# Kernel tuning notes

Hardware: AMD Instinct MI355X
Metric: run time of the kernel (lower is better)

The kernel has to match this reference:

```python
import jax, jax.numpy as jnp
import numpy as np

B, L, D = 16, 1024, 512
EPS = 1e-6


def setup_inputs() -> dict:
    key = jax.random.key(0)
    ks = jax.random.split(key, 12)
    inp = {
        'q': jax.random.normal(ks[0], (B, L, D), jnp.float32),
        'k': jax.random.normal(ks[1], (B, L, D), jnp.float32),
        'v': jax.random.normal(ks[2], (B, L, D), jnp.float32),
        'inputs_lengths': jax.random.randint(ks[3], (B,), 1, L + 1),
        'distance_matrix': jax.random.uniform(ks[4], (B, L, L), jnp.float32),
        'Wq': jax.random.normal(ks[5], (D, D), jnp.float32) / np.sqrt(D),
        'Wk': jax.random.normal(ks[6], (D, D), jnp.float32) / np.sqrt(D),
        'Wv': jax.random.normal(ks[7], (D, D), jnp.float32) / np.sqrt(D),
        'Wqt': jax.random.normal(ks[8], (D, D), jnp.float32) / np.sqrt(D),
        'Wkt': jax.random.normal(ks[9], (D, D), jnp.float32) / np.sqrt(D),
        'Wfc': jax.random.normal(ks[10], (D, D), jnp.float32) / np.sqrt(D),
        'gamma': jnp.ones((D,), jnp.float32),
        'beta': jnp.zeros((D,), jnp.float32),
    }
    return inp


def reference(q, k, v, inputs_lengths, distance_matrix, Wq, Wk, Wv, Wqt, Wkt, Wfc, gamma, beta):
    temperature = jnp.asarray(D, q.dtype) ** 0.5
    residual = q
    # projections (torch Linear: x @ W.T)
    qp = jnp.einsum('bld,ed->ble', q, Wq)
    kp = jnp.einsum('bld,ed->ble', k, Wk)
    vp = jnp.einsum('bld,ed->ble', v, Wv)
    qt = jnp.einsum('bld,ed->ble', q, Wqt)
    kt = jnp.einsum('bld,ed->ble', k, Wkt)
    # distance-weighted time features: [B,L,L] @ [B,L,D]
    qt = jnp.einsum('blm,bmd->bld', distance_matrix, qt)
    kt = jnp.einsum('blm,bmd->bld', distance_matrix, kt)
    # scores: content + distance term
    attn = jnp.einsum('bld,bmd->blm', qp / temperature, kp)
    attn = attn + jnp.einsum('bld,bmd->blm', qt / temperature, kt)
    # pad_zero_masking: zero out key positions beyond each sequence length
    mask = (jnp.arange(L)[None, :] < inputs_lengths[:, None]).astype(attn.dtype)  # [B, L]
    mask = mask[:, None, :]  # [B, 1, L] broadcast over query dim
    attn = jnp.tanh(attn * mask) * mask
    out = jnp.einsum('blm,bmd->bld', attn, vp)
    out = jnp.einsum('bld,ed->ble', out, Wfc) + residual
    # LayerNorm(eps=1e-6)
    mu = jnp.mean(out, axis=-1, keepdims=True)
    var = jnp.mean((out - mu) ** 2, axis=-1, keepdims=True)
    out = (out - mu) * jax.lax.rsqrt(var + EPS) * gamma + beta
    return (out, attn)
```

## Files before the change

kernel.cpp:

```cpp
#include <hip/hip_runtime.h>
#include <math.h>

#define LL 1024
#define DD 512
#define NB 16

typedef __attribute__((ext_vector_type(8))) short bf16x8;
typedef __attribute__((ext_vector_type(4))) float f32x4;
typedef unsigned short u16;
typedef unsigned int u32;
typedef const __attribute__((address_space(1))) void* gptr_t;
typedef __attribute__((address_space(3))) void* sptr_t;

static const long NLD = (long)NB * LL * DD;
static const long NLL = (long)NB * LL * LL;

__device__ __forceinline__ u16 f2bf(float x) {
  u32 u = __float_as_uint(x);
  u += 0x7fffu + ((u >> 16) & 1u);
  return (u16)(u >> 16);
}
__device__ __forceinline__ float bf2f(u16 h) {
  return __uint_as_float((u32)h << 16);
}

__global__ __launch_bounds__(256) void k_split3(
    const float* __restrict__ q, const float* __restrict__ k,
    const float* __restrict__ v, u16* __restrict__ qh, u16* __restrict__ ql,
    u16* __restrict__ kh, u16* __restrict__ kl, u16* __restrict__ vh) {
  const int z = blockIdx.z;
  const float* x = (z == 0) ? q : (z == 1) ? k : v;
  u16* hi = (z == 0) ? qh : (z == 1) ? kh : vh;
  u16* lo = (z == 0) ? ql : kl;
  const long stride = (long)gridDim.x * 1024;
  for (long i = ((long)blockIdx.x * 256 + threadIdx.x) * 4; i < NLD;
       i += stride) {
    const float4 vv = *(const float4*)(x + i);
    ushort4 h;
    h.x = f2bf(vv.x);
    h.y = f2bf(vv.y);
    h.z = f2bf(vv.z);
    h.w = f2bf(vv.w);
    *(ushort4*)(hi + i) = h;
    if (z < 2) {
      ushort4 s;
      s.x = f2bf(vv.x - bf2f(h.x));
      s.y = f2bf(vv.y - bf2f(h.y));
      s.z = f2bf(vv.z - bf2f(h.z));
      s.w = f2bf(vv.w - bf2f(h.w));
      *(ushort4*)(lo + i) = s;
    }
  }
}

__global__ __launch_bounds__(256) void k_splitd(const float* __restrict__ x,
                                                u16* __restrict__ hi,
                                                u16* __restrict__ lo) {
  const long stride = (long)gridDim.x * 1024;
  for (long i = ((long)blockIdx.x * 256 + threadIdx.x) * 4; i < NLL;
       i += stride) {
    const float4 v = *(const float4*)(x + i);
    ushort4 h, s;
    h.x = f2bf(v.x);
    h.y = f2bf(v.y);
    h.z = f2bf(v.z);
    h.w = f2bf(v.w);
    s.x = f2bf(v.x - bf2f(h.x));
    s.y = f2bf(v.y - bf2f(h.y));
    s.z = f2bf(v.z - bf2f(h.z));
    s.w = f2bf(v.w - bf2f(h.w));
    *(ushort4*)(hi + i) = h;
    *(ushort4*)(lo + i) = s;
  }
}

__global__ __launch_bounds__(256) void k_splitw(
    const float* __restrict__ Wq, const float* __restrict__ Wk,
    const float* __restrict__ Wv, const float* __restrict__ Wfc,
    const float* __restrict__ Wqt, const float* __restrict__ Wkt,
    u16* __restrict__ Wq_h, u16* __restrict__ Wk_h, u16* __restrict__ Wv_h,
    u16* __restrict__ Wfc_h, u16* __restrict__ Wqt_h,
    u16* __restrict__ Wqt_l, u16* __restrict__ Wkt_h,
    u16* __restrict__ Wkt_l) {
  const int z = blockIdx.z;
  const float* x;
  u16 *hi, *lo = nullptr;
  switch (z) {
    case 0: x = Wq; hi = Wq_h; break;
    case 1: x = Wk; hi = Wk_h; break;
    case 2: x = Wv; hi = Wv_h; break;
    case 3: x = Wfc; hi = Wfc_h; break;
    case 4: x = Wqt; hi = Wqt_h; lo = Wqt_l; break;
    default: x = Wkt; hi = Wkt_h; lo = Wkt_l; break;
  }
  const long i = ((long)blockIdx.x * 256 + threadIdx.x) * 4;
  const float4 v = *(const float4*)(x + i);
  ushort4 h;
  h.x = f2bf(v.x);
  h.y = f2bf(v.y);
  h.z = f2bf(v.z);
  h.w = f2bf(v.w);
  *(ushort4*)(hi + i) = h;
  if (z >= 4) {
    ushort4 s;
    s.x = f2bf(v.x - bf2f(h.x));
    s.y = f2bf(v.y - bf2f(h.y));
    s.z = f2bf(v.z - bf2f(h.z));
    s.w = f2bf(v.w - bf2f(h.w));
    *(ushort4*)(lo + i) = s;
  }
}

template <int NISS>
__device__ __forceinline__ void stage_tile(const u16* __restrict__ G, long ld,
                                           int row0, int k0, char* lds, int w,
                                           int l) {
#pragma unroll
  for (int i = 0; i < NISS; ++i) {
    const int off = i * 4096 + w * 1024 + l * 16;
    const int r = off >> 6;
    const int cp = (off >> 4) & 3;
    const int c = cp ^ ((r >> 1) & 3);
    __builtin_amdgcn_global_load_lds(
        (gptr_t)(G + (long)(row0 + r) * ld + k0 + c * 8),
        (sptr_t)(lds + i * 4096 + w * 1024), 16, 0, 0);
  }
}

__device__ __forceinline__ bf16x8 read_frag(const char* lds, int r, int ks) {
  const int cp = ks ^ ((r >> 1) & 3);
  return *(const bf16x8*)(lds + r * 64 + cp * 16);
}

__device__ __forceinline__ void core_plain(const u16* __restrict__ A, long lda,
                                           const u16* __restrict__ B, long ldb,
                                           int K, int bm, int bn, char* smem,
                                           f32x4 acc[4][4]) {
  const int tid = threadIdx.x, w = tid >> 6, l = tid & 63;
  const int wm = (w >> 1) * 64, wn = (w & 1) * 64;
  const int fr = l & 15, ks = l >> 4;
  char* As = smem;
  char* Bs = smem + 8192;
  for (int k0 = 0; k0 < K; k0 += 32) {
    stage_tile<2>(A, lda, bm, k0, As, w, l);
    stage_tile<2>(B, ldb, bn, k0, Bs, w, l);
    __syncthreads();
    bf16x8 af[4], bg[4];
#pragma unroll
    for (int i = 0; i < 4; ++i) {
      af[i] = read_frag(As, wm + i * 16 + fr, ks);
      bg[i] = read_frag(Bs, wn + i * 16 + fr, ks);
    }
#pragma unroll
    for (int mi = 0; mi < 4; ++mi)
#pragma unroll
      for (int ni = 0; ni < 4; ++ni)
        acc[mi][ni] = __builtin_amdgcn_mfma_f32_16x16x32_bf16(
            af[mi], bg[ni], acc[mi][ni], 0, 0, 0);
    __syncthreads();
  }
}

__device__ __forceinline__ void core_split(
    const u16* __restrict__ Ah, const u16* __restrict__ Al, long lda,
    const u16* __restrict__ Bh, const u16* __restrict__ Bl, long ldb, int K,
    int bm, int bn, char* smem, f32x4 acc[4][4]) {
  const int tid = threadIdx.x, w = tid >> 6, l = tid & 63;
  const int wm = (w >> 1) * 64, wn = (w & 1) * 64;
  const int fr = l & 15, ks = l >> 4;
  char* Ash = smem;
  char* Bsh = smem + 8192;
  char* Asl = smem + 16384;
  char* Bsl = smem + 24576;
  for (int k0 = 0; k0 < K; k0 += 32) {
    stage_tile<2>(Ah, lda, bm, k0, Ash, w, l);
    stage_tile<2>(Bh, ldb, bn, k0, Bsh, w, l);
    stage_tile<2>(Al, lda, bm, k0, Asl, w, l);
    stage_tile<2>(Bl, ldb, bn, k0, Bsl, w, l);
    __syncthreads();
    bf16x8 ah[4], bh[4];
#pragma unroll
    for (int i = 0; i < 4; ++i) {
      ah[i] = read_frag(Ash, wm + i * 16 + fr, ks);
      bh[i] = read_frag(Bsh, wn + i * 16 + fr, ks);
    }
#pragma unroll
    for (int mi = 0; mi < 4; ++mi)
#pragma unroll
      for (int ni = 0; ni < 4; ++ni)
        acc[mi][ni] = __builtin_amdgcn_mfma_f32_16x16x32_bf16(
            ah[mi], bh[ni], acc[mi][ni], 0, 0, 0);
    bf16x8 bl[4];
#pragma unroll
    for (int ni = 0; ni < 4; ++ni)
      bl[ni] = read_frag(Bsl, wn + ni * 16 + fr, ks);
#pragma unroll
    for (int mi = 0; mi < 4; ++mi)
#pragma unroll
      for (int ni = 0; ni < 4; ++ni)
        acc[mi][ni] = __builtin_amdgcn_mfma_f32_16x16x32_bf16(
            ah[mi], bl[ni], acc[mi][ni], 0, 0, 0);
    bf16x8 al[4];
#pragma unroll
    for (int mi = 0; mi < 4; ++mi)
      al[mi] = read_frag(Asl, wm + mi * 16 + fr, ks);
#pragma unroll
    for (int mi = 0; mi < 4; ++mi)
#pragma unroll
      for (int ni = 0; ni < 4; ++ni)
        acc[mi][ni] = __builtin_amdgcn_mfma_f32_16x16x32_bf16(
            al[mi], bh[ni], acc[mi][ni], 0, 0, 0);
    __syncthreads();
  }
}

#define EPI_PROLOG()                                       \
  const int tid = threadIdx.x, w = tid >> 6, l = tid & 63; \
  const int wm = (w >> 1) * 64, wn = (w & 1) * 64;         \
  const int fr = l & 15, ks = l >> 4;

__global__ __launch_bounds__(256, 3) void k_proj_p(
    const u16* __restrict__ q_hi, const u16* __restrict__ k_hi,
    const u16* __restrict__ v_hi, const u16* __restrict__ Wq_h,
    const u16* __restrict__ Wk_h, const u16* __restrict__ Wv_h,
    const int* __restrict__ lens, u16* __restrict__ qp, u16* __restrict__ kp,
    u16* __restrict__ vp) {
  const int bm = blockIdx.y * 128, bn = blockIdx.x * 128;
  const u16 *A, *B;
  u16* C;
  switch (blockIdx.z) {
    case 0: A = q_hi; B = Wq_h; C = qp; break;
    case 1: A = k_hi; B = Wk_h; C = kp; break;
    default: A = v_hi; B = Wv_h; C = vp; break;
  }
  if (blockIdx.z != 0) {
    const int len = lens[bm >> 10];
    if ((bm & 1023) >= len) return;
  }
  __shared__ __align__(16) char smem[16384];
  f32x4 acc[4][4] = {};
  core_plain(A, DD, B, DD, DD, bm, bn, smem, acc);
  EPI_PROLOG()
#pragma unroll
  for (int mi = 0; mi < 4; ++mi) {
    const int R0 = bm + wm + mi * 16 + ks * 4;
#pragma unroll
    for (int ni = 0; ni < 4; ++ni) {
      const int col = bn + wn + ni * 16 + fr;
#pragma unroll
      for (int j = 0; j < 4; ++j)
        C[(long)(R0 + j) * DD + col] = f2bf(acc[mi][ni][j]);
    }
  }
}

__global__ __launch_bounds__(256, 3) void k_proj_t(
    const u16* __restrict__ q_hi, const u16* __restrict__ q_lo,
    const u16* __restrict__ k_hi, const u16* __restrict__ k_lo,
    const u16* __restrict__ Wqt_h, const u16* __restrict__ Wqt_l,
    const u16* __restrict__ Wkt_h, const u16* __restrict__ Wkt_l,
    u16* __restrict__ qt0h, u16* __restrict__ qt0l, u16* __restrict__ kt0h,
    u16* __restrict__ kt0l) {
  const int sel = blockIdx.z;
  const u16* Ah = sel ? k_hi : q_hi;
  const u16* Al = sel ? k_lo : q_lo;
  const u16* Bh = sel ? Wkt_h : Wqt_h;
  const u16* Bl = sel ? Wkt_l : Wqt_l;
  u16* Ch = sel ? kt0h : qt0h;
  u16* Cl = sel ? kt0l : qt0l;
  __shared__ __align__(16) char smem[32768];
  const int bm = blockIdx.y * 128, bn = blockIdx.x * 128;
  f32x4 acc[4][4] = {};
  core_split(Ah, Al, DD, Bh, Bl, DD, DD, bm, bn, smem, acc);
  EPI_PROLOG()
#pragma unroll
  for (int mi = 0; mi < 4; ++mi) {
    const int R0 = bm + wm + mi * 16 + ks * 4;
#pragma unroll
    for (int ni = 0; ni < 4; ++ni) {
      const int col = bn + wn + ni * 16 + fr;
#pragma unroll
      for (int j = 0; j < 4; ++j) {
        const long idx = (long)(R0 + j) * DD + col;
        const float x = acc[mi][ni][j];
        const u16 h = f2bf(x);
        Ch[idx] = h;
        Cl[idx] = f2bf(x - bf2f(h));
      }
    }
  }
}

__global__ __launch_bounds__(256) void k_tr(
    const u16* __restrict__ qt0h, const u16* __restrict__ qt0l,
    const u16* __restrict__ kt0h, const u16* __restrict__ kt0l,
    const u16* __restrict__ vp, const int* __restrict__ lens,
    u16* __restrict__ qTh, u16* __restrict__ qTl, u16* __restrict__ kTh,
    u16* __restrict__ kTl, u16* __restrict__ vpT) {
  const int z = blockIdx.z;
  const int b = z / 5, s = z - b * 5;
  const int r0 = blockIdx.y * 64, c0 = blockIdx.x * 64;
  if (s == 4 && r0 >= lens[b]) return;
  const u16* X;
  u16* O;
  switch (s) {
    case 0: X = qt0h; O = qTh; break;
    case 1: X = qt0l; O = qTl; break;
    case 2: X = kt0h; O = kTh; break;
    case 3: X = kt0l; O = kTl; break;
    default: X = vp; O = vpT; break;
  }
  X += (long)b * LL * DD;
  O += (long)b * LL * DD;
  __shared__ u16 t[64][68];
  const int tid = threadIdx.x;
#pragma unroll
  for (int i = 0; i < 16; ++i) {
    const int idx = tid + i * 256;
    t[idx >> 6][idx & 63] = X[(long)(r0 + (idx >> 6)) * DD + c0 + (idx & 63)];
  }
  __syncthreads();
#pragma unroll
  for (int i = 0; i < 16; ++i) {
    const int idx = tid + i * 256;
    const int rr = idx >> 6, cc = idx & 63;
    O[(long)(c0 + rr) * LL + r0 + cc] = t[cc][rr];
  }
}

__global__ __launch_bounds__(256, 3) void k_dist_g(
    const u16* __restrict__ dist_h, const u16* __restrict__ dist_l,
    const u16* __restrict__ qT_h, const u16* __restrict__ qT_l,
    const u16* __restrict__ kT_h, const u16* __restrict__ kT_l,
    const int* __restrict__ lens, u16* __restrict__ qt_h,
    u16* __restrict__ qt_l, u16* __restrict__ kt_h, u16* __restrict__ kt_l) {
  const int flat = blockIdx.x + (blockIdx.y << 2) + (blockIdx.z << 5);
  const int swz = ((flat & 7) << 7) | (flat >> 3);
  const int bn = (swz & 3) << 7;
  const int bm = ((swz >> 2) & 7) << 7;
  const int zz = swz >> 5;
  const int b = zz >> 1, sel = zz & 1;
  if (sel == 1 && bm >= lens[b]) return;
  const u16* Ah = dist_h + (long)b * LL * LL;
  const u16* Al = dist_l + (long)b * LL * LL;
  const u16* Bh = (sel ? kT_h : qT_h) + (long)b * LL * DD;
  const u16* Bl = (sel ? kT_l : qT_l) + (long)b * LL * DD;
  u16* Oh = (sel ? kt_h : qt_h) + (long)b * LL * DD;
  u16* Ol = (sel ? kt_l : qt_l) + (long)b * LL * DD;
  __shared__ __align__(16) char smem[32768];
  f32x4 acc[4][4] = {};
  core_split(Ah, Al, LL, Bh, Bl, LL, LL, bm, bn, smem, acc);
  EPI_PROLOG()
#pragma unroll
  for (int mi = 0; mi < 4; ++mi) {
    const int R0 = bm + wm + mi * 16 + ks * 4;
#pragma unroll
    for (int ni = 0; ni < 4; ++ni) {
      const int col = bn + wn + ni * 16 + fr;
#pragma unroll
      for (int j = 0; j < 4; ++j) {
        const long idx = (long)(R0 + j) * DD + col;
        const float x = acc[mi][ni][j];
        const u16 h = f2bf(x);
        Oh[idx] = h;
        Ol[idx] = f2bf(x - bf2f(h));
      }
    }
  }
}

__global__ __launch_bounds__(256, 3) void k_score(
    const u16* __restrict__ qp, const u16* __restrict__ kp,
    const u16* __restrict__ qt_h, const u16* __restrict__ qt_l,
    const u16* __restrict__ kt_h, const u16* __restrict__ kt_l,
    const int* __restrict__ lens, float* __restrict__ attnF,
    u16* __restrict__ attnB) {
  const int flat = blockIdx.x + (blockIdx.y << 3) + (blockIdx.z << 6);
  const int swz = ((flat & 7) << 7) | (flat >> 3);
  const int bn = (swz & 7) << 7;
  const int bm = ((swz >> 3) & 7) << 7;
  const int b = swz >> 6;
  const int len = lens[b];
  const int tid = threadIdx.x;
  const long baseF = (long)b * LL * LL;
  if (bn >= len) {
    const float4 zf = make_float4(0.f, 0.f, 0.f, 0.f);
    const ushort4 zh = {0, 0, 0, 0};
    for (int i = tid; i < 4096; i += 256) {
      const int row = i >> 5, c = (i & 31) << 2;
      const long idx = baseF + (long)(bm + row) * LL + bn + c;
      *(float4*)&attnF[idx] = zf;
      *(ushort4*)&attnB[idx] = zh;
    }
    return;
  }
  const long od = (long)b * LL * DD;
  const u16* Ah = qt_h + od;
  const u16* Al = qt_l + od;
  const u16* Bh = kt_h + od;
  const u16* Bl = kt_l + od;
  const u16* Ap = qp + od;
  const u16* Bp = kp + od;
  __shared__ __align__(16) char smem[49152];
  char* Ash = smem;
  char* Bsh = smem + 8192;
  char* Asl = smem + 16384;
  char* Bsl = smem + 24576;
  char* Aps = smem + 32768;
  char* Bps = smem + 40960;
  const int w = tid >> 6, l = tid & 63;
  const int wm = (w >> 1) * 64, wn = (w & 1) * 64;
  const int fr = l & 15, ks = l >> 4;
  f32x4 acc[4][4] = {};
  for (int k0 = 0; k0 < DD; k0 += 32) {
    stage_tile<2>(Ah, DD, bm, k0, Ash, w, l);
    stage_tile<2>(Bh, DD, bn, k0, Bsh, w, l);
    stage_tile<2>(Al, DD, bm, k0, Asl, w, l);
    stage_tile<2>(Bl, DD, bn, k0, Bsl, w, l);
    stage_tile<2>(Ap, DD, bm, k0, Aps, w, l);
    stage_tile<2>(Bp, DD, bn, k0, Bps, w, l);
    __syncthreads();
    bf16x8 ah[4], bh[4];
#pragma unroll
    for (int i = 0; i < 4; ++i) {
      ah[i] = read_frag(Ash, wm + i * 16 + fr, ks);
      bh[i] = read_frag(Bsh, wn + i * 16 + fr, ks);
    }
#pragma unroll
    for (int mi = 0; mi < 4; ++mi)
#pragma unroll
      for (int ni = 0; ni < 4; ++ni)
        acc[mi][ni] = __builtin_amdgcn_mfma_f32_16x16x32_bf16(
            ah[mi], bh[ni], acc[mi][ni], 0, 0, 0);
    bf16x8 bl[4];
#pragma unroll
    for (int ni = 0; ni < 4; ++ni)
      bl[ni] = read_frag(Bsl, wn + ni * 16 + fr, ks);
#pragma unroll
    for (int mi = 0; mi < 4; ++mi)
#pragma unroll
      for (int ni = 0; ni < 4; ++ni)
        acc[mi][ni] = __builtin_amdgcn_mfma_f32_16x16x32_bf16(
            ah[mi], bl[ni], acc[mi][ni], 0, 0, 0);
    bf16x8 al[4];
#pragma unroll
    for (int mi = 0; mi < 4; ++mi)
      al[mi] = read_frag(Asl, wm + mi * 16 + fr, ks);
#pragma unroll
    for (int mi = 0; mi < 4; ++mi)
#pragma unroll
      for (int ni = 0; ni < 4; ++ni)
        acc[mi][ni] = __builtin_amdgcn_mfma_f32_16x16x32_bf16(
            al[mi], bh[ni], acc[mi][ni], 0, 0, 0);
    bf16x8 ap[4], bp[4];
#pragma unroll
    for (int i = 0; i < 4; ++i) {
      ap[i] = read_frag(Aps, wm + i * 16 + fr, ks);
      bp[i] = read_frag(Bps, wn + i * 16 + fr, ks);
    }
#pragma unroll
    for (int mi = 0; mi < 4; ++mi)
#pragma unroll
      for (int ni = 0; ni < 4; ++ni)
        acc[mi][ni] = __builtin_amdgcn_mfma_f32_16x16x32_bf16(
            ap[mi], bp[ni], acc[mi][ni], 0, 0, 0);
    __syncthreads();
  }
  const float invt = 0.04419417382415922f;
#pragma unroll
  for (int mi = 0; mi < 4; ++mi) {
    const int R0 = bm + wm + mi * 16 + ks * 4;
#pragma unroll
    for (int ni = 0; ni < 4; ++ni) {
      const int col = bn + wn + ni * 16 + fr;
      const float m = (col < len) ? 1.0f : 0.0f;
#pragma unroll
      for (int j = 0; j < 4; ++j) {
        const float s = tanhf(acc[mi][ni][j] * invt * m) * m;
        const long idx = baseF + (long)(R0 + j) * LL + col;
        attnF[idx] = s;
        attnB[idx] = f2bf(s);
      }
    }
  }
}

__global__ __launch_bounds__(256, 3) void k_pv(const u16* __restrict__ attnB,
                                               const u16* __restrict__ vpT,
                                               const int* __restrict__ lens,
                                               u16* __restrict__ out0) {
  const int b = blockIdx.z;
  const int Kt = ((lens[b] + 31) >> 5) << 5;
  __shared__ __align__(16) char smem[16384];
  const int bm = blockIdx.y * 128, bn = blockIdx.x * 128;
  f32x4 acc[4][4] = {};
  core_plain(attnB + (long)b * LL * LL, LL, vpT + (long)b * LL * DD, LL, Kt,
             bm, bn, smem, acc);
  u16* C = out0 + (long)b * LL * DD;
  EPI_PROLOG()
#pragma unroll
  for (int mi = 0; mi < 4; ++mi) {
    const int R0 = bm + wm + mi * 16 + ks * 4;
#pragma unroll
    for (int ni = 0; ni < 4; ++ni) {
      const int col = bn + wn + ni * 16 + fr;
#pragma unroll
      for (int j = 0; j < 4; ++j)
        C[(long)(R0 + j) * DD + col] = f2bf(acc[mi][ni][j]);
    }
  }
}

__global__ __launch_bounds__(256, 2) void k_fcln(
    const u16* __restrict__ out0, const u16* __restrict__ Wfc_h,
    const float* __restrict__ q, const float* __restrict__ gamma,
    const float* __restrict__ beta, float* __restrict__ outO) {
  __shared__ __align__(16) char smem[36864];
  __shared__ float red[2][64][5];
  const int tid = threadIdx.x, w = tid >> 6, l = tid & 63;
  const int wn = w * 128;
  const int fr = l & 15, ks = l >> 4;
  const int bm = blockIdx.x * 64;
  char* As = smem;
  char* Bs = smem + 4096;
  f32x4 acc[4][8] = {};
  for (int k0 = 0; k0 < DD; k0 += 32) {
    stage_tile<1>(out0, DD, bm, k0, As, w, l);
    stage_tile<8>(Wfc_h, DD, 0, k0, Bs, w, l);
    __syncthreads();
    bf16x8 af[4], bg[8];
#pragma unroll
    for (int mi = 0; mi < 4; ++mi) af[mi] = read_frag(As, mi * 16 + fr, ks);
#pragma unroll
    for (int ni = 0; ni < 8; ++ni)
      bg[ni] = read_frag(Bs, wn + ni * 16 + fr, ks);
#pragma unroll
    for (int mi = 0; mi < 4; ++mi)
#pragma unroll
      for (int ni = 0; ni < 8; ++ni)
        acc[mi][ni] = __builtin_amdgcn_mfma_f32_16x16x32_bf16(
            af[mi], bg[ni], acc[mi][ni], 0, 0, 0);
    __syncthreads();
  }
  float p1[4][4], p2[4][4];
#pragma unroll
  for (int mi = 0; mi < 4; ++mi)
#pragma unroll
    for (int j = 0; j < 4; ++j) {
      p1[mi][j] = 0.0f;
      p2[mi][j] = 0.0f;
    }
#pragma unroll
  for (int mi = 0; mi < 4; ++mi) {
    const int r = mi * 16 + ks * 4;
#pragma unroll
    for (int ni = 0; ni < 8; ++ni) {
      const int col = wn + ni * 16 + fr;
#pragma unroll
      for (int j = 0; j < 4; ++j) {
        const float val = acc[mi][ni][j] + q[(long)(bm + r + j) * DD + col];
        acc[mi][ni][j] = val;
        p1[mi][j] += val;
        p2[mi][j] += val * val;
      }
    }
  }
#pragma unroll
  for (int off = 1; off < 16; off <<= 1) {
#pragma unroll
    for (int mi = 0; mi < 4; ++mi)
#pragma unroll
      for (int j = 0; j < 4; ++j) {
        p1[mi][j] += __shfl_xor(p1[mi][j], off);
        p2[mi][j] += __shfl_xor(p2[mi][j], off);
      }
  }
  if (fr == 0) {
#pragma unroll
    for (int mi = 0; mi < 4; ++mi)
#pragma unroll
      for (int j = 0; j < 4; ++j) {
        red[0][mi * 16 + ks * 4 + j][w] = p1[mi][j];
        red[1][mi * 16 + ks * 4 + j][w] = p2[mi][j];
      }
  }
  __syncthreads();
#pragma unroll
  for (int mi = 0; mi < 4; ++mi) {
#pragma unroll
    for (int j = 0; j < 4; ++j) {
      const int r = mi * 16 + ks * 4 + j;
      const float s1 =
          red[0][r][0] + red[0][r][1] + red[0][r][2] + red[0][r][3];
      const float s2 =
          red[1][r][0] + red[1][r][1] + red[1][r][2] + red[1][r][3];
      const float mu = s1 * (1.0f / DD);
      const float rs = rsqrtf(s2 * (1.0f / DD) - mu * mu + 1e-6f);
#pragma unroll
      for (int ni = 0; ni < 8; ++ni) {
        const int col = wn + ni * 16 + fr;
        outO[(long)(bm + r) * DD + col] =
            (acc[mi][ni][j] - mu) * rs * gamma[col] + beta[col];
      }
    }
  }
}

extern "C" void kernel_launch(void* const* d_in, const int* in_sizes, int n_in,
                              void* d_out, int out_size, void* d_ws,
                              size_t ws_size, hipStream_t stream) {
  const float* q = (const float*)d_in[0];
  const float* k = (const float*)d_in[1];
  const float* v = (const float*)d_in[2];
  const int* lens = (const int*)d_in[3];
  const float* dist = (const float*)d_in[4];
  const float* Wq = (const float*)d_in[5];
  const float* Wk = (const float*)d_in[6];
  const float* Wv = (const float*)d_in[7];
  const float* Wqt = (const float*)d_in[8];
  const float* Wkt = (const float*)d_in[9];
  const float* Wfc = (const float*)d_in[10];
  const float* gamma = (const float*)d_in[11];
  const float* beta = (const float*)d_in[12];

  char* W = (char*)d_ws;
  const size_t SB = 16777216;
  u16* q_hi = (u16*)(W + 0 * SB);
  u16* q_lo = (u16*)(W + 1 * SB);
  u16* k_hi = (u16*)(W + 2 * SB);
  u16* k_lo = (u16*)(W + 3 * SB);
  u16* v_hi = (u16*)(W + 4 * SB);
  u16* dist_h = (u16*)(W + 5 * SB);
  u16* dist_l = (u16*)(W + 7 * SB);
  u16* qp_bf = (u16*)(W + 9 * SB);
  u16* kp_bf = (u16*)(W + 10 * SB);
  u16* vp_bf = (u16*)(W + 11 * SB);
  u16* qt0h = (u16*)(W + 12 * SB);
  u16* qt0l = (u16*)(W + 13 * SB);
  u16* kt0h = (u16*)(W + 14 * SB);
  u16* kt0l = (u16*)(W + 15 * SB);
  u16* qT_h = (u16*)(W + 16 * SB);
  u16* qT_l = (u16*)(W + 17 * SB);
  u16* kT_h = (u16*)(W + 18 * SB);
  u16* kT_l = (u16*)(W + 19 * SB);
  char* WB = W + 20 * SB;
  const size_t WS = 524288;
  u16* Wq_h = (u16*)(WB + 0 * WS);
  u16* Wk_h = (u16*)(WB + 1 * WS);
  u16* Wv_h = (u16*)(WB + 2 * WS);
  u16* Wfc_h = (u16*)(WB + 3 * WS);
  u16* Wqt_h = (u16*)(WB + 4 * WS);
  u16* Wqt_l = (u16*)(WB + 5 * WS);
  u16* Wkt_h = (u16*)(WB + 6 * WS);
  u16* Wkt_l = (u16*)(WB + 7 * WS);
  u16* qt_h = q_hi;
  u16* qt_l = q_lo;
  u16* kt_h = k_hi;
  u16* kt_l = k_lo;
  u16* vpT = v_hi;
  u16* attnB = dist_h;
  u16* out0 = qp_bf;

  float* outO = (float*)d_out;
  float* attnF = outO + NLD;

  dim3 blk(256);
  k_split3<<<dim3(1024, 1, 3), blk, 0, stream>>>(q, k, v, q_hi, q_lo, k_hi,
                                                 k_lo, v_hi);
  k_splitd<<<4096, blk, 0, stream>>>(dist, dist_h, dist_l);
  k_splitw<<<dim3(256, 1, 6), blk, 0, stream>>>(Wq, Wk, Wv, Wfc, Wqt, Wkt,
                                                Wq_h, Wk_h, Wv_h, Wfc_h,
                                                Wqt_h, Wqt_l, Wkt_h, Wkt_l);

  k_proj_p<<<dim3(4, 128, 3), blk, 0, stream>>>(q_hi, k_hi, v_hi, Wq_h, Wk_h,
                                                Wv_h, lens, qp_bf, kp_bf,
                                                vp_bf);
  k_proj_t<<<dim3(4, 128, 2), blk, 0, stream>>>(q_hi, q_lo, k_hi, k_lo, Wqt_h,
                                                Wqt_l, Wkt_h, Wkt_l, qt0h,
                                                qt0l, kt0h, kt0l);
  k_tr<<<dim3(8, 16, 80), blk, 0, stream>>>(qt0h, qt0l, kt0h, kt0l, vp_bf,
                                            lens, qT_h, qT_l, kT_h, kT_l,
                                            vpT);
  k_dist_g<<<dim3(4, 8, 32), blk, 0, stream>>>(dist_h, dist_l, qT_h, qT_l,
                                               kT_h, kT_l, lens, qt_h, qt_l,
                                               kt_h, kt_l);
  k_score<<<dim3(8, 8, 16), blk, 0, stream>>>(qp_bf, kp_bf, qt_h, qt_l, kt_h,
                                              kt_l, lens, attnF, attnB);
  k_pv<<<dim3(4, 8, 16), blk, 0, stream>>>(attnB, vpT, lens, out0);
  k_fcln<<<dim3(256), blk, 0, stream>>>(out0, Wfc_h, q, gamma, beta, outO);
}
```

Baseline: 453.9 us.

## Compact block grids by scanning lengths so active tiles dispatch first

Replaces 3D grids with flat 1D grids in which block indices are mapped through a prefix scan over sequence lengths. Tiles that do real work are packed at the front and masked-out tiles are either placed last (zero-fill in the score kernel) or map to early-exit blocks. In the dist and pv kernels the batch index becomes the fastest-varying dimension. This aims to cut wasted early-exit blocks and improve load balance across CUs. The cost is a serial 16-iteration scan per block, and the previous L2-friendly swizzle is dropped.

```diff
diff --git a/kernel.cpp b/kernel.cpp
--- a/kernel.cpp
+++ b/kernel.cpp
@@ -219,23 +219,53 @@
   const int wm = (w >> 1) * 64, wn = (w & 1) * 64;         \
   const int fr = l & 15, ks = l >> 4;
 
+__device__ __forceinline__ int scan_batches(const int* __restrict__ lens,
+                                            int e, int mult, int* loc,
+                                            int* rem) {
+  for (int i = 0; i < NB; ++i) {
+    const int c = mult * ((lens[i] + 127) >> 7);
+    if (e < c) {
+      *loc = e;
+      return i;
+    }
+    e -= c;
+  }
+  *rem = e;
+  return -1;
+}
+
 __global__ __launch_bounds__(256, 3) void k_proj_p(
     const u16* __restrict__ q_hi, const u16* __restrict__ k_hi,
     const u16* __restrict__ v_hi, const u16* __restrict__ Wq_h,
     const u16* __restrict__ Wk_h, const u16* __restrict__ Wv_h,
     const int* __restrict__ lens, u16* __restrict__ qp, u16* __restrict__ kp,
     u16* __restrict__ vp) {
-  const int bm = blockIdx.y * 128, bn = blockIdx.x * 128;
+  const int flat = blockIdx.x;
   const u16 *A, *B;
   u16* C;
-  switch (blockIdx.z) {
-    case 0: A = q_hi; B = Wq_h; C = qp; break;
-    case 1: A = k_hi; B = Wk_h; C = kp; break;
-    default: A = v_hi; B = Wv_h; C = vp; break;
-  }
-  if (blockIdx.z != 0) {
-    const int len = lens[bm >> 10];
-    if ((bm & 1023) >= len) return;
+  int bm, bn;
+  if (flat < 512) {
+    A = q_hi;
+    B = Wq_h;
+    C = qp;
+    bm = (flat >> 2) * 128;
+    bn = (flat & 3) * 128;
+  } else {
+    int loc, rem;
+    int b = scan_batches(lens, flat - 512, 4, &loc, &rem);
+    if (b >= 0) {
+      A = k_hi;
+      B = Wk_h;
+      C = kp;
+    } else {
+      b = scan_batches(lens, rem, 4, &loc, &rem);
+      if (b < 0) return;
+      A = v_hi;
+      B = Wv_h;
+      C = vp;
+    }
+    bm = b * 1024 + (loc >> 2) * 128;
+    bn = (loc & 3) * 128;
   }
   __shared__ __align__(16) char smem[16384];
   f32x4 acc[4][4] = {};
@@ -334,13 +364,22 @@
     const u16* __restrict__ kT_h, const u16* __restrict__ kT_l,
     const int* __restrict__ lens, u16* __restrict__ qt_h,
     u16* __restrict__ qt_l, u16* __restrict__ kt_h, u16* __restrict__ kt_l) {
-  const int flat = blockIdx.x + (blockIdx.y << 2) + (blockIdx.z << 5);
-  const int swz = ((flat & 7) << 7) | (flat >> 3);
-  const int bn = (swz & 3) << 7;
-  const int bm = ((swz >> 2) & 7) << 7;
-  const int zz = swz >> 5;
-  const int b = zz >> 1, sel = zz & 1;
-  if (sel == 1 && bm >= lens[b]) return;
+  const int flat = blockIdx.x;
+  int b, sel, bm, bn;
+  if (flat < 512) {
+    sel = 0;
+    b = flat & 15;
+    const int r = flat >> 4;
+    bm = (r >> 2) * 128;
+    bn = (r & 3) * 128;
+  } else {
+    int loc, rem;
+    b = scan_batches(lens, flat - 512, 4, &loc, &rem);
+    if (b < 0) return;
+    sel = 1;
+    bm = (loc >> 2) * 128;
+    bn = (loc & 3) * 128;
+  }
   const u16* Ah = dist_h + (long)b * LL * LL;
   const u16* Al = dist_l + (long)b * LL * LL;
   const u16* Bh = (sel ? kT_h : qT_h) + (long)b * LL * DD;
@@ -375,15 +414,25 @@
     const u16* __restrict__ kt_h, const u16* __restrict__ kt_l,
     const int* __restrict__ lens, float* __restrict__ attnF,
     u16* __restrict__ attnB) {
-  const int flat = blockIdx.x + (blockIdx.y << 3) + (blockIdx.z << 6);
-  const int swz = ((flat & 7) << 7) | (flat >> 3);
-  const int bn = (swz & 7) << 7;
-  const int bm = ((swz >> 3) & 7) << 7;
-  const int b = swz >> 6;
-  const int len = lens[b];
   const int tid = threadIdx.x;
-  const long baseF = (long)b * LL * LL;
-  if (bn >= len) {
+  int loc, rem;
+  int b = scan_batches(lens, blockIdx.x, 8, &loc, &rem);
+  int bm, bn;
+  if (b < 0) {
+    for (int i = 0; i < NB; ++i) {
+      const int nbn = (lens[i] + 127) >> 7;
+      const int c = (8 - nbn) << 3;
+      if (rem < c) {
+        b = i;
+        const int wdt = 8 - nbn;
+        bm = (rem / wdt) * 128;
+        bn = (nbn + rem % wdt) * 128;
+        break;
+      }
+      rem -= c;
+    }
+    if (b < 0) return;
+    const long baseF = (long)b * LL * LL;
     const float4 zf = make_float4(0.f, 0.f, 0.f, 0.f);
     const ushort4 zh = {0, 0, 0, 0};
     for (int i = tid; i < 4096; i += 256) {
@@ -394,6 +443,11 @@
     }
     return;
   }
+  const int nbn = (lens[b] + 127) >> 7;
+  bm = (loc / nbn) * 128;
+  bn = (loc % nbn) * 128;
+  const int len = lens[b];
+  const long baseF = (long)b * LL * LL;
   const long od = (long)b * LL * DD;
   const u16* Ah = qt_h + od;
   const u16* Al = qt_l + od;
@@ -489,10 +543,12 @@
                                                const u16* __restrict__ vpT,
                                                const int* __restrict__ lens,
                                                u16* __restrict__ out0) {
-  const int b = blockIdx.z;
+  const int flat = blockIdx.x;
+  const int b = flat & 15;
+  const int r = flat >> 4;
+  const int bm = (r >> 2) * 128, bn = (r & 3) * 128;
   const int Kt = ((lens[b] + 31) >> 5) << 5;
   __shared__ __align__(16) char smem[16384];
-  const int bm = blockIdx.y * 128, bn = blockIdx.x * 128;
   f32x4 acc[4][4] = {};
   core_plain(attnB + (long)b * LL * LL, LL, vpT + (long)b * LL * DD, LL, Kt,
              bm, bn, smem, acc);
@@ -672,20 +728,18 @@
                                                 Wq_h, Wk_h, Wv_h, Wfc_h,
                                                 Wqt_h, Wqt_l, Wkt_h, Wkt_l);
 
-  k_proj_p<<<dim3(4, 128, 3), blk, 0, stream>>>(q_hi, k_hi, v_hi, Wq_h, Wk_h,
-                                                Wv_h, lens, qp_bf, kp_bf,
-                                                vp_bf);
+  k_proj_p<<<1536, blk, 0, stream>>>(q_hi, k_hi, v_hi, Wq_h, Wk_h, Wv_h, lens,
+                                     qp_bf, kp_bf, vp_bf);
   k_proj_t<<<dim3(4, 128, 2), blk, 0, stream>>>(q_hi, q_lo, k_hi, k_lo, Wqt_h,
                                                 Wqt_l, Wkt_h, Wkt_l, qt0h,
                                                 qt0l, kt0h, kt0l);
   k_tr<<<dim3(8, 16, 80), blk, 0, stream>>>(qt0h, qt0l, kt0h, kt0l, vp_bf,
                                             lens, qT_h, qT_l, kT_h, kT_l,
                                             vpT);
-  k_dist_g<<<dim3(4, 8, 32), blk, 0, stream>>>(dist_h, dist_l, qT_h, qT_l,
-                                               kT_h, kT_l, lens, qt_h, qt_l,
-                                               kt_h, kt_l);
-  k_score<<<dim3(8, 8, 16), blk, 0, stream>>>(qp_bf, kp_bf, qt_h, qt_l, kt_h,
-                                              kt_l, lens, attnF, attnB);
-  k_pv<<<dim3(4, 8, 16), blk, 0, stream>>>(attnB, vpT, lens, out0);
-  k_fcln<<<dim3(256), blk, 0, stream>>>(out0, Wfc_h, q, gamma, beta, outO);
-}
+  k_dist_g<<<1024, blk, 0, stream>>>(dist_h, dist_l, qT_h, qT_l, kT_h, kT_l,
+                                     lens, qt_h, qt_l, kt_h, kt_l);
+  k_score<<<1024, blk, 0, stream>>>(qp_bf, kp_bf, qt_h, qt_l, kt_h, kt_l,
+                                    lens, attnF, attnB);
+  k_pv<<<512, blk, 0, stream>>>(attnB, vpT, lens, out0);
+  k_fcln<<<256, blk, 0, stream>>>(out0, Wfc_h, q, gamma, beta, outO);
+}
```

Result: no change. 458.7 us (+1.1%).
